# Kernel tuning notes

Hardware: AMD Instinct MI355X
Metric: run time of the kernel (lower is better)

## Reference

```python
import jax, jax.numpy as jnp
import numpy as np

H, L, N1, N2, N3 = 256, 141, 9, 34, 98
B, S = 64, 512

def setup_inputs() -> dict:
    key = jax.random.key(0)
    cnt = [0]
    def nrm(shape, s=0.05):
        cnt[0] += 1
        return jax.random.normal(jax.random.fold_in(key, cnt[0]), shape, jnp.float32) * s
    d = {}
    d['inputs'] = jax.random.randint(jax.random.fold_in(key, 1000), (B, S), 0, 30522)
    d['text_hidden'] = nrm((B, S, 768), 1.0)
    d['label_encoding'] = nrm((L, H), 1.0)
    d['w12'] = (jax.random.uniform(jax.random.fold_in(key, 1001), (N1, N2)) < 0.3).astype(jnp.float32)
    d['w23'] = (jax.random.uniform(jax.random.fold_in(key, 1002), (N2, N3)) < 0.3).astype(jnp.float32)
    d['fre12'] = jax.random.uniform(jax.random.fold_in(key, 1003), (N1, N2), jnp.float32)
    d['fre23'] = jax.random.uniform(jax.random.fold_in(key, 1004), (N2, N3), jnp.float32)
    for name in ['wi1', 'wf1', 'wo1', 'wu1', 'wi2', 'wf2', 'wo2', 'wu2']:
        d[name + '_W'] = nrm((H, H)); d[name + '_b'] = nrm((H,))
    for name in ['ui1', 'uf1', 'uo1', 'uu1', 'ui2', 'uf2', 'uo2', 'uu2']:
        d[name + '_W'] = nrm((H, H))
    d['mix_W'] = nrm((3 * H, H)); d['mix_b'] = nrm((H,))
    d['tt_W'] = nrm((768, H)); d['tt_b'] = nrm((H,))
    d['A'] = nrm((L, L)); d['Wp'] = nrm((H, H))
    d['out_W'] = nrm((L * H, L)); d['out_b'] = nrm((L,))
    return d

def reference(inputs, text_hidden, label_encoding, w12, w23, fre12, fre23,
              wi1_W, wi1_b, wf1_W, wf1_b, wo1_W, wo1_b, wu1_W, wu1_b,
              wi2_W, wi2_b, wf2_W, wf2_b, wo2_W, wo2_b, wu2_W, wu2_b,
              ui1_W, uf1_W, uo1_W, uu1_W, ui2_W, uf2_W, uo2_W, uu2_W,
              mix_W, mix_b, tt_W, tt_b, A, Wp, out_W, out_b):
    sig, tanh = jax.nn.sigmoid, jnp.tanh
    v1 = label_encoding[:N1]          # [N1,H]
    v2 = label_encoding[N1:N1 + N2]   # [N2,H]
    v3 = label_encoding[N1 + N2:]     # [N3,H]
    w21, w32 = w12.T, w23.T
    # --- top-down tree-LSTM (suffix 1) ---
    i11 = sig(v1 @ wi1_W + wi1_b); o11 = sig(v1 @ wo1_W + wo1_b); u11 = tanh(v1 @ wu1_W + wu1_b)
    c11 = i11 * u11; h11 = o11 * tanh(c11)
    h21t = w21 @ h11
    i21 = sig(v2 @ wi1_W + wi1_b + h21t @ ui1_W)
    f21 = sig(v2 @ wf1_W + wf1_b + h21t @ uf1_W)
    o21 = sig(v2 @ wo1_W + wo1_b + h21t @ uo1_W)
    u21 = tanh(v2 @ wu1_W + wu1_b + h21t @ uu1_W)
    c21 = i21 * u21 + f21 * (w21 @ c11); h21 = o21 * tanh(c21)
    h31t = w32 @ h21
    i31 = sig(v3 @ wi1_W + wi1_b + h31t @ ui1_W)
    f31 = sig(v3 @ wf1_W + wf1_b + h31t @ uf1_W)
    o31 = sig(v3 @ wo1_W + wo1_b + h31t @ uo1_W)
    u31 = tanh(v3 @ wu1_W + wu1_b + h31t @ uu1_W)
    c31 = i31 * u31 + f31 * (w32 @ c21); h31 = o31 * tanh(c31)
    # --- bottom-up tree-LSTM (suffix 2) ---
    i32 = sig(v3 @ wi2_W + wi2_b); o32 = sig(v3 @ wo2_W + wo2_b); u32 = tanh(v3 @ wu2_W + wu2_b)
    c32 = i32 * u32; h32 = o32 * tanh(c32)
    h22t = fre23 @ h32
    i22 = sig(v2 @ wi2_W + wi2_b + h22t @ ui2_W)
    f22 = sig((w32 @ v2) @ wf2_W + wf2_b + h32 @ uf2_W)   # [N3,H]
    o22 = sig(v2 @ wo2_W + wo2_b + h22t @ uo2_W)
    u22 = tanh(v2 @ wu2_W + wu2_b + h22t @ uu2_W)
    c22 = i22 * u22 + w23 @ (f22 * c32); h22 = o22 * tanh(c22)
    h12t = fre12 @ h22
    i12 = sig(v1 @ wi2_W + wi2_b + h12t @ ui2_W)
    f12 = sig((w21 @ v1) @ wf2_W + wf2_b + h22 @ uf2_W)   # [N2,H]
    o12 = sig(v1 @ wo2_W + wo2_b + h12t @ uo2_W)
    u12 = tanh(v1 @ wu2_W + wu2_b + h12t @ uu2_W)
    c12 = i12 * u12 + w12 @ (f12 * c22); h12 = o12 * tanh(c12)
    h1 = jnp.concatenate([h11, h12], axis=1)
    h2 = jnp.concatenate([h21, h22], axis=1)
    h3 = jnp.concatenate([h31, h32], axis=1)
    le = jnp.concatenate([h1, h2, h3], axis=0)            # [L,2H]
    temp = jax.nn.relu(A @ label_encoding @ Wp)           # [L,H]
    le = jnp.concatenate([le, temp], axis=1) @ mix_W + mix_b  # [L,H]
    # --- masked cross-attention pooling over text ---
    text = tanh(text_hidden @ tt_W + tt_b)                # [B,S,H]
    att = jnp.einsum('lh,bsh->bls', le, text)             # [B,L,S]
    pad = jnp.where((inputs == 0) | (inputs == 101) | (inputs == 102), -jnp.inf, 0.0).astype(text.dtype)
    att = jax.nn.softmax(att + pad[:, None, :], axis=2)
    features = jnp.einsum('bls,bsh->blh', att, text).reshape(inputs.shape[0], -1)  # [B,L*H]
    return sig(features @ out_W + out_b)                  # [B,L]
```

## Files before the change

kernel.cpp:

```cpp
#include <hip/hip_runtime.h>
#include <math.h>

static constexpr int H = 256, L = 141, N1 = 9, N2 = 34, N3 = 98;
static constexpr int B = 64, S = 512;

typedef __attribute__((ext_vector_type(8))) _Float16 f16x8;
typedef __attribute__((ext_vector_type(4))) float f32x4;

__device__ inline unsigned short f2h(float x) {
    _Float16 h = (_Float16)x;
    return __builtin_bit_cast(unsigned short, h);
}
__device__ inline float sigf(float x) { return 1.f / (1.f + __expf(-x)); }

__device__ inline void gload_lds16(const void* g, void* l) {
    __builtin_amdgcn_global_load_lds(
        (const __attribute__((address_space(1))) void*)g,
        (__attribute__((address_space(3))) void*)l, 16, 0, 0);
}

__device__ inline f16x8 cvt8(float4 lo, float4 hi) {
    union { unsigned int u[4]; f16x8 v; } r;
    r.u[0] = f2h(lo.x) | ((unsigned int)f2h(lo.y) << 16);
    r.u[1] = f2h(lo.z) | ((unsigned int)f2h(lo.w) << 16);
    r.u[2] = f2h(hi.x) | ((unsigned int)f2h(hi.y) << 16);
    r.u[3] = f2h(hi.z) | ((unsigned int)f2h(hi.w) << 16);
    return r.v;
}

__global__ __launch_bounds__(256) void conv_ttW(
    const float* __restrict__ W, unsigned short* __restrict__ Bt)
{
    __shared__ unsigned short Tl[32][257];
    const int t = blockIdx.x, tid = threadIdx.x;
    #pragma unroll
    for (int p = 0; p < 32; p++) {
        int lin = p * 256 + tid;
        int r = lin >> 8, c = lin & 255;
        Tl[r][c] = f2h(W[(long)(t * 32 + r) * 256 + c]);
    }
    __syncthreads();
    unsigned short v[32];
    #pragma unroll
    for (int kin = 0; kin < 32; kin++) v[kin] = Tl[kin][tid];
    uint4* dst = (uint4*)(Bt + ((long)t * 256 + tid) * 32);
    #pragma unroll
    for (int q = 0; q < 4; q++) dst[q] = ((const uint4*)v)[q];
}

__global__ __launch_bounds__(256) void text_gemm2(
    const float* __restrict__ Af,
    const unsigned short* __restrict__ Bt,
    const float* __restrict__ bias,
    unsigned short* __restrict__ outH,
    unsigned short* __restrict__ outHT)
{
    __shared__ unsigned short T[256 * 72];
    const int tid  = threadIdx.x;
    const int wave = tid >> 6, lane = tid & 63;
    const int quad = lane >> 4, l16 = lane & 15;
    const int m0 = blockIdx.x * 64;
    const int wm = (wave & 1) * 32;
    const int wn = (wave >> 1) * 128;

    const float* ap0 = Af + (long)(m0 + wm + l16) * 768 + quad * 8;
    const float* ap1 = ap0 + 16 * 768;
    const unsigned short* bp = Bt + (wn + l16) * 32 + quad * 8;

    f32x4 acc[2][8] = {};
    uint4  br0[8], br1[8];
    float4 ar0[4], ar1[4];

    auto tg_load = [&](int tt, uint4 (&BR)[8], float4 (&AR)[4]) {
        const unsigned short* bq = bp + (long)tt * 8192;
        #pragma unroll
        for (int j = 0; j < 8; j++) BR[j] = *(const uint4*)(bq + j * 512);
        const float* a0 = ap0 + tt * 32;
        const float* a1 = ap1 + tt * 32;
        AR[0] = *(const float4*)a0;
        AR[1] = *(const float4*)(a0 + 4);
        AR[2] = *(const float4*)a1;
        AR[3] = *(const float4*)(a1 + 4);
    };
    auto tg_comp = [&](const uint4 (&BR)[8], const float4 (&AR)[4]) {
        f16x8 a0 = cvt8(AR[0], AR[1]);
        f16x8 a1 = cvt8(AR[2], AR[3]);
        #pragma unroll
        for (int j = 0; j < 8; j++) {
            f16x8 bj = __builtin_bit_cast(f16x8, BR[j]);
            acc[0][j] = __builtin_amdgcn_mfma_f32_16x16x32_f16(a0, bj, acc[0][j], 0, 0, 0);
            acc[1][j] = __builtin_amdgcn_mfma_f32_16x16x32_f16(a1, bj, acc[1][j], 0, 0, 0);
        }
    };

    tg_load(0, br0, ar0);
    #pragma unroll 1
    for (int t = 0; t < 24; t += 2) {
        tg_load(t + 1, br1, ar1);
        tg_comp(br0, ar0);
        if (t + 2 < 24) tg_load(t + 2, br0, ar0);
        tg_comp(br1, ar1);
    }

    float bv[8];
    #pragma unroll
    for (int j = 0; j < 8; j++) bv[j] = bias[wn + j * 16 + l16];

    #pragma unroll
    for (int i = 0; i < 2; i++) {
        #pragma unroll
        for (int j = 0; j < 8; j++) {
            const int mlb = wm + i * 16 + quad * 4;
            const int n   = wn + j * 16 + l16;
            unsigned short hv[4];
            #pragma unroll
            for (int r = 0; r < 4; r++) {
                float v = tanhf(acc[i][j][r] + bv[j]);
                hv[r] = f2h(v);
                outH[(long)(m0 + mlb + r) * 256 + n] = hv[r];
            }
            uint2 p;
            p.x = hv[0] | ((unsigned int)hv[1] << 16);
            p.y = hv[2] | ((unsigned int)hv[3] << 16);
            *(uint2*)&T[n * 72 + mlb] = p;
        }
    }
    __syncthreads();
    {
        const int bb = m0 >> 9, s0 = m0 & 511;
        uint4* dst = (uint4*)&outHT[((long)bb * 256 + tid) * 512 + s0];
        const uint4* src = (const uint4*)&T[tid * 72];
        #pragma unroll
        for (int q = 0; q < 8; q++) dst[q] = src[q];
    }
}

template<int EPI, bool CONVA, int IM>
__global__ __launch_bounds__(256) void gemm_mfma(
    const void* __restrict__ Aptr, int lda, long strA,
    const unsigned short* __restrict__ Bp, int ldb, long strB,
    float* __restrict__ C, int ldc, long strC,
    int M, int N, int K,
    const float* __restrict__ bias,
    const int* __restrict__ tokens,
    unsigned short* __restrict__ outH,
    unsigned short* __restrict__ outHT,
    int kChunk)
{
    __shared__ unsigned short A_s[32 * IM * 32];
    __shared__ unsigned short B_s[128 * 32];
    __shared__ unsigned short T[EPI == 1 ? 128 * 64 : 1];
    const int tid  = threadIdx.x;
    const int wave = tid >> 6, lane = tid & 63;
    const int quad = lane >> 4, l16 = lane & 15;
    const int bz = blockIdx.z;
    const int m0 = blockIdx.y * (32 * IM), n0 = blockIdx.x * 128;
    const int wm = (wave & 1) * (16 * IM), wn = (wave >> 1) * 64;

    long aBase, bBase;
    int kBeg, kEnd;
    if (EPI == 4) { aBase = 0; bBase = 0; kBeg = bz * kChunk; kEnd = kBeg + kChunk; }
    else { aBase = (long)bz * strA; bBase = (long)bz * strB; kBeg = 0; kEnd = K; }

    f32x4 acc[IM][4] = {};

    for (int k0 = kBeg; k0 < kEnd; k0 += 32) {
        if (CONVA) {
            const float* Af = (const float*)Aptr + aBase;
            #pragma unroll
            for (int it = 0; it < IM; it++) {
                int idx = it * 256 + tid;
                int row = idx >> 3, col4 = idx & 7;
                int gm = m0 + row; if (gm > M - 1) gm = M - 1;
                float4 v = *(const float4*)(Af + (long)gm * lda + k0 + col4 * 4);
                unsigned int p0 = f2h(v.x) | ((unsigned int)f2h(v.y) << 16);
                unsigned int p1 = f2h(v.z) | ((unsigned int)f2h(v.w) << 16);
                *(uint2*)&A_s[row * 32 + col4 * 4] = make_uint2(p0, p1);
            }
        } else {
            const unsigned short* Ab = (const unsigned short*)Aptr + aBase;
            #pragma unroll
            for (int t = 0; t < IM / 2; t++) {
                int rowb = wave * (8 * IM) + t * 16;
                int gm = m0 + rowb + (lane >> 2); if (gm > M - 1) gm = M - 1;
                gload_lds16(Ab + (long)gm * lda + k0 + (lane & 3) * 8,
                            &A_s[rowb * 32]);
            }
        }
        #pragma unroll
        for (int t = 0; t < 2; t++) {
            int rowb = wave * 32 + t * 16;
            int gn = n0 + rowb + (lane >> 2); if (gn > N - 1) gn = N - 1;
            gload_lds16(Bp + bBase + (long)gn * ldb + k0 + (lane & 3) * 8,
                        &B_s[rowb * 32]);
        }
        __syncthreads();
        f16x8 a[IM], b[4];
        #pragma unroll
        for (int i = 0; i < IM; i++)
            a[i] = *(const f16x8*)&A_s[(wm + i * 16 + l16) * 32 + quad * 8];
        #pragma unroll
        for (int j = 0; j < 4; j++)
            b[j] = *(const f16x8*)&B_s[(wn + j * 16 + l16) * 32 + quad * 8];
        #pragma unroll
        for (int i = 0; i < IM; i++)
            #pragma unroll
            for (int j = 0; j < 4; j++)
                acc[i][j] = __builtin_amdgcn_mfma_f32_16x16x32_f16(
                    a[i], b[j], acc[i][j], 0, 0, 0);
        __syncthreads();
    }

    #pragma unroll
    for (int i = 0; i < IM; i++) {
        #pragma unroll
        for (int j = 0; j < 4; j++) {
            #pragma unroll
            for (int r = 0; r < 4; r++) {
                int ml = wm + i * 16 + quad * 4 + r;
                int nl = wn + j * 16 + l16;
                int gm = m0 + ml, gn = n0 + nl;
                if (gm >= M || gn >= N) continue;
                float v = acc[i][j][r];
                if (EPI == 1) {
                    v = tanhf(v + bias[gn]);
                    unsigned short hv = f2h(v);
                    outH[(long)gm * ldc + gn] = hv;
                    T[nl * 64 + ml] = hv;
                } else if (EPI == 2) {
                    int tok = tokens[(long)bz * 512 + gn];
                    if (tok == 0 || tok == 101 || tok == 102) v -= 1e30f;
                    C[(long)bz * strC + (long)gm * ldc + gn] = v;
                } else if (EPI == 3) {
                    outH[(long)bz * strC + (long)gm * ldc + gn] = f2h(v);
                } else {
                    C[(long)bz * strC + (long)gm * ldc + gn] = v;
                }
            }
        }
    }
    if (EPI == 1) {
        __syncthreads();
        int bb = m0 >> 9, s0 = m0 & 511;
        int rr = tid >> 1, half = tid & 1;
        const uint4* srcp = (const uint4*)&T[rr * 64 + half * 32];
        uint4* dstp = (uint4*)&outHT[((long)bb * 256 + n0 + rr) * 512 + s0 + half * 32];
        dstp[0] = srcp[0]; dstp[1] = srcp[1]; dstp[2] = srcp[2]; dstp[3] = srcp[3];
    }
}

__global__ __launch_bounds__(256) void transp_t64(
    const float* __restrict__ src, unsigned short* __restrict__ dst,
    int R, int C)
{
    __shared__ unsigned short T[64 * 65];
    const int tid = threadIdx.x;
    const int r0 = blockIdx.x * 64, c0 = blockIdx.y * 64;
    #pragma unroll
    for (int p = 0; p < 16; p++) {
        int lin = p * 256 + tid;
        int r = lin >> 6, c = lin & 63;
        int gc = c0 + c;
        float v = (gc < C) ? src[(long)(r0 + r) * C + gc] : 0.f;
        T[c * 65 + r] = f2h(v);
    }
    __syncthreads();
    #pragma unroll
    for (int p = 0; p < 16; p++) {
        int lin = p * 256 + tid;
        int c = lin >> 6, r = lin & 63;
        if (c0 + c < C)
            dst[(long)(c0 + c) * R + r0 + r] = T[c * 65 + r];
    }
}

__global__ __launch_bounds__(256) void gate_pre(
    const float* __restrict__ le,
    const float* W0, const float* W1, const float* W2, const float* W3,
    const float* W4, const float* W5, const float* W6,
    const float* b0, const float* b1, const float* b2, const float* b3,
    const float* b4, const float* b5, const float* b6,
    float* __restrict__ G)
{
    __shared__ float ls[256];
    __shared__ float red[256];
    const int j = blockIdx.x >> 2, x = blockIdx.x & 3, m = blockIdx.y;
    const int tid = threadIdx.x, nl = tid & 63, ks = tid >> 6, n = x * 64 + nl;
    ls[tid] = le[(long)m * 256 + tid];
    __syncthreads();
    const float *W, *bb;
    switch (j) {
        case 0: W = W0; bb = b0; break;  case 1: W = W1; bb = b1; break;
        case 2: W = W2; bb = b2; break;  case 3: W = W3; bb = b3; break;
        case 4: W = W4; bb = b4; break;  case 5: W = W5; bb = b5; break;
        default: W = W6; bb = b6;
    }
    float a0 = 0, a1 = 0, a2 = 0, a3 = 0;
    for (int k = ks; k + 12 < 256; k += 16) {
        long o = (long)k * 256 + n;
        a0 += ls[k] * W[o];        a1 += ls[k + 4] * W[o + 1024];
        a2 += ls[k + 8] * W[o + 2048]; a3 += ls[k + 12] * W[o + 3072];
    }
    red[tid] = a0 + a1 + a2 + a3;
    __syncthreads();
    if (ks == 0)
        G[((long)j * 141 + m) * 256 + n] =
            red[nl] + red[64 + nl] + red[128 + nl] + red[192 + nl] + bb[n];
}

__global__ __launch_bounds__(256) void pre2(
    const float* __restrict__ A, const float* __restrict__ le,
    const float* __restrict__ w23, const float* __restrict__ w12,
    const float* __restrict__ Wp, const float* __restrict__ wf2_W,
    float* __restrict__ tmpP, float* __restrict__ wv2f, float* __restrict__ wv1f)
{
    __shared__ float cs[141];
    __shared__ float t[256];
    __shared__ float red[256];
    const int x = blockIdx.x, y = blockIdx.y;
    const int tid = threadIdx.x, nl = tid & 63, ks = tid >> 6, n = x * 64 + nl;
    int job, m, K1;
    if (y < 141)      { job = 0; m = y;       K1 = 141; }
    else if (y < 239) { job = 1; m = y - 141; K1 = 34; }
    else              { job = 2; m = y - 239; K1 = 9; }
    if (tid < K1)
        cs[tid] = (job == 0) ? A[(long)m * 141 + tid]
                : (job == 1) ? w23[(long)tid * 98 + m]
                             : w12[(long)tid * 34 + m];
    __syncthreads();
    const float* s1 = (job == 1) ? le + 9 * 256 : le;
    float acc = 0;
    #pragma unroll 4
    for (int k = 0; k < K1; k++) acc += cs[k] * s1[(long)k * 256 + tid];
    t[tid] = acc;
    __syncthreads();
    const float* W = (job == 0) ? Wp : wf2_W;
    float a0 = 0, a1 = 0, a2 = 0, a3 = 0;
    for (int k = ks; k + 12 < 256; k += 16) {
        long o = (long)k * 256 + n;
        a0 += t[k] * W[o];        a1 += t[k + 4] * W[o + 1024];
        a2 += t[k + 8] * W[o + 2048]; a3 += t[k + 12] * W[o + 3072];
    }
    red[tid] = a0 + a1 + a2 + a3;
    __syncthreads();
    if (ks == 0) {
        float tot = red[nl] + red[64 + nl] + red[128 + nl] + red[192 + nl];
        if (job == 0)      tmpP[(long)m * 256 + n] = fmaxf(tot, 0.f);
        else if (job == 1) wv2f[(long)m * 256 + n] = tot;
        else               wv1f[(long)m * 256 + n] = tot;
    }
}

__global__ __launch_bounds__(256) void ew1(
    const float* __restrict__ G, float* __restrict__ h11, float* __restrict__ c11,
    float* __restrict__ h32, float* __restrict__ c32)
{
    int y = blockIdx.x, n = threadIdx.x;
    if (y < 9) {
        int m = y;
        float iv = sigf(G[(0L * 141 + m) * 256 + n]);
        float ov = sigf(G[(2L * 141 + m) * 256 + n]);
        float uv = tanhf(G[(3L * 141 + m) * 256 + n]);
        float cv = iv * uv;
        c11[m * 256 + n] = cv; h11[m * 256 + n] = ov * tanhf(cv);
    } else {
        int r = y - 9, grow = 43 + r;
        float iv = sigf(G[(4L * 141 + grow) * 256 + n]);
        float ov = sigf(G[(5L * 141 + grow) * 256 + n]);
        float uv = tanhf(G[(6L * 141 + grow) * 256 + n]);
        float cv = iv * uv;
        c32[r * 256 + n] = cv; h32[r * 256 + n] = ov * tanhf(cv);
    }
}

__global__ __launch_bounds__(256) void chain_mm(int phase,
    const float* __restrict__ w12, const float* __restrict__ w23,
    const float* __restrict__ fre23, const float* __restrict__ fre12,
    const float* __restrict__ h11, const float* __restrict__ c11,
    const float* __restrict__ h32,
    const float* __restrict__ h21, const float* __restrict__ c21,
    const float* __restrict__ h22,
    const float* __restrict__ wv2f, const float* __restrict__ wv1f,
    const float* __restrict__ wf2_b, const float* __restrict__ uf2_W,
    const float* __restrict__ c32, const float* __restrict__ c22,
    float* __restrict__ h21t, float* __restrict__ c21p,
    float* __restrict__ h22t, float* __restrict__ fcb,
    float* __restrict__ h31t, float* __restrict__ c31p,
    float* __restrict__ h12t, float* __restrict__ fc2b)
{
    __shared__ float cs[256];
    __shared__ float red[256];
    const int x = blockIdx.x, y = blockIdx.y;
    const int tid = threadIdx.x, nl = tid & 63, ks = tid >> 6, n = x * 64 + nl;
    int job, m;
    if (phase == 0) {
        if (y < 34)       { job = 0; m = y; }
        else if (y < 68)  { job = 1; m = y - 34; }
        else if (y < 102) { job = 2; m = y - 68; }
        else              { job = 3; m = y - 102; }
    } else {
        if (y < 98)       { job = 0; m = y; }
        else if (y < 196) { job = 1; m = y - 98; }
        else if (y < 205) { job = 2; m = y - 196; }
        else              { job = 3; m = y - 205; }
    }
    if (job < 3) {
        int K; const float* src; float* dst;
        if (phase == 0) {
            K = (job == 2) ? 98 : 9;
            src = (job == 0) ? h11 : (job == 1) ? c11 : h32;
            dst = (job == 0) ? h21t : (job == 1) ? c21p : h22t;
            if (tid < K)
                cs[tid] = (job == 2) ? fre23[(long)m * 98 + tid]
                                     : w12[(long)tid * 34 + m];
        } else {
            K = 34;
            src = (job == 0) ? h21 : (job == 1) ? c21 : h22;
            dst = (job == 0) ? h31t : (job == 1) ? c31p : h12t;
            if (tid < K)
                cs[tid] = (job == 2) ? fre12[(long)m * 34 + tid]
                                     : w23[(long)tid * 98 + m];
        }
        __syncthreads();
        float a0 = 0;
        for (int k = ks; k < K; k += 4) a0 += cs[k] * src[(long)k * 256 + n];
        red[tid] = a0;
        __syncthreads();
        if (ks == 0)
            dst[(long)m * 256 + n] = red[nl] + red[64 + nl] + red[128 + nl] + red[192 + nl];
    } else {
        const float* row = (phase == 0) ? h32 + m * 256 : h22 + m * 256;
        const float* pre = (phase == 0) ? wv2f : wv1f;
        const float* cm  = (phase == 0) ? c32 : c22;
        float* dst       = (phase == 0) ? fcb : fc2b;
        cs[tid] = row[tid];
        __syncthreads();
        float a0 = 0, a1 = 0, a2 = 0, a3 = 0;
        for (int k = ks; k + 12 < 256; k += 16) {
            long o = (long)k * 256 + n;
            a0 += cs[k] * uf2_W[o];        a1 += cs[k + 4] * uf2_W[o + 1024];
            a2 += cs[k + 8] * uf2_W[o + 2048]; a3 += cs[k + 12] * uf2_W[o + 3072];
        }
        red[tid] = a0 + a1 + a2 + a3;
        __syncthreads();
        if (ks == 0) {
            float tot = red[nl] + red[64 + nl] + red[128 + nl] + red[192 + nl]
                      + pre[(long)m * 256 + n] + wf2_b[n];
            dst[(long)m * 256 + n] = sigf(tot) * cm[(long)m * 256 + n];
        }
    }
}

__global__ __launch_bounds__(256) void lstm_fused(int phase,
    const float* __restrict__ G,
    const float* __restrict__ h21t, const float* __restrict__ c21p,
    const float* __restrict__ h22t, const float* __restrict__ fcb,
    const float* __restrict__ h31t, const float* __restrict__ c31p,
    const float* __restrict__ h12t, const float* __restrict__ fc2b,
    const float* __restrict__ w23, const float* __restrict__ w12,
    const float* __restrict__ ui1, const float* __restrict__ uf1,
    const float* __restrict__ uo1, const float* __restrict__ uu1,
    const float* __restrict__ ui2, const float* __restrict__ uo2,
    const float* __restrict__ uu2,
    float* __restrict__ h21, float* __restrict__ c21,
    float* __restrict__ h22, float* __restrict__ c22,
    float* __restrict__ h31, float* __restrict__ h12)
{
    __shared__ float hs[256];
    __shared__ float cs[128];
    __shared__ float red[1024];
    const int x = blockIdx.x, y = blockIdx.y;
    const int tid = threadIdx.x, nl = tid & 63, ks = tid >> 6, n = x * 64 + nl;
    bool modef; int m, grow, Kx = 0;
    const float *hrow, *U0, *U1, *U2, *U3 = nullptr, *Sx = nullptr, *cmod = nullptr;
    float *ho, *co = nullptr;
    if (phase == 0) {
        if (y < 34) { modef = true;  m = y;      grow = 9 + m;  hrow = h21t;
                      U0 = ui1; U1 = uf1; U2 = uo1; U3 = uu1; cmod = c21p; ho = h21; co = c21; }
        else        { modef = false; m = y - 34; grow = 9 + m;  hrow = h22t;
                      U0 = ui2; U1 = uo2; U2 = uu2; Sx = fcb; Kx = 98; ho = h22; co = c22;
                      if (tid < 98) cs[tid] = w23[(long)m * 98 + tid]; }
    } else {
        if (y < 98) { modef = true;  m = y;      grow = 43 + m; hrow = h31t;
                      U0 = ui1; U1 = uf1; U2 = uo1; U3 = uu1; cmod = c31p; ho = h31; co = nullptr; }
        else        { modef = false; m = y - 98; grow = m;      hrow = h12t;
                      U0 = ui2; U1 = uo2; U2 = uu2; Sx = fc2b; Kx = 34; ho = h12; co = nullptr;
                      if (tid < 34) cs[tid] = w12[(long)m * 34 + tid]; }
    }
    hs[tid] = hrow[(long)m * 256 + tid];
    __syncthreads();
    float a0 = 0, a1 = 0, a2 = 0, a3 = 0;
    if (modef) {
        for (int k = ks; k < 256; k += 4) {
            float xv = hs[k]; long o = (long)k * 256 + n;
            a0 += xv * U0[o]; a1 += xv * U1[o]; a2 += xv * U2[o]; a3 += xv * U3[o];
        }
    } else {
        for (int k = ks; k < 256; k += 4) {
            float xv = hs[k]; long o = (long)k * 256 + n;
            a0 += xv * U0[o]; a1 += xv * U1[o]; a2 += xv * U2[o];
        }
        for (int k = ks; k < Kx; k += 4) a3 += cs[k] * Sx[(long)k * 256 + n];
    }
    red[tid] = a0; red[256 + tid] = a1; red[512 + tid] = a2; red[768 + tid] = a3;
    __syncthreads();
    if (ks == 0) {
        float t0 = 0, t1 = 0, t2 = 0, t3 = 0;
        #pragma unroll
        for (int s2 = 0; s2 < 4; s2++) {
            t0 += red[s2 * 64 + nl];       t1 += red[256 + s2 * 64 + nl];
            t2 += red[512 + s2 * 64 + nl]; t3 += red[768 + s2 * 64 + nl];
        }
        if (modef) {
            float ti = t0 + G[(0L * 141 + grow) * 256 + n];
            float tf = t1 + G[(1L * 141 + grow) * 256 + n];
            float to = t2 + G[(2L * 141 + grow) * 256 + n];
            float tu = t3 + G[(3L * 141 + grow) * 256 + n];
            float cv = sigf(ti) * tanhf(tu) + sigf(tf) * cmod[(long)m * 256 + n];
            ho[(long)m * 256 + n] = sigf(to) * tanhf(cv);
            if (co) co[(long)m * 256 + n] = cv;
        } else {
            float ti = t0 + G[(4L * 141 + grow) * 256 + n];
            float to = t1 + G[(5L * 141 + grow) * 256 + n];
            float tu = t2 + G[(6L * 141 + grow) * 256 + n];
            float cv = sigf(ti) * tanhf(tu) + t3;
            ho[(long)m * 256 + n] = sigf(to) * tanhf(cv);
            if (co) co[(long)m * 256 + n] = cv;
        }
    }
}

__global__ __launch_bounds__(256) void mix_mm(
    const float* __restrict__ h11, const float* __restrict__ h12,
    const float* __restrict__ h21, const float* __restrict__ h22,
    const float* __restrict__ h31, const float* __restrict__ h32,
    const float* __restrict__ tmpP, const float* __restrict__ mix_W,
    const float* __restrict__ mix_b, unsigned short* __restrict__ le_h)
{
    __shared__ float ls[768];
    __shared__ float red[256];
    const int x = blockIdx.x, l = blockIdx.y;
    const int tid = threadIdx.x, nl = tid & 63, ks = tid >> 6, n = x * 64 + nl;
    const float *pa, *pb; int r;
    if (l < 9)       { pa = h11; pb = h12; r = l; }
    else if (l < 43) { pa = h21; pb = h22; r = l - 9; }
    else             { pa = h31; pb = h32; r = l - 43; }
    for (int j = tid; j < 768; j += 256) {
        float v;
        if (j < 256)      v = pa[r * 256 + j];
        else if (j < 512) v = pb[r * 256 + (j - 256)];
        else              v = tmpP[l * 256 + (j - 512)];
        ls[j] = v;
    }
    __syncthreads();
    float a0 = 0, a1 = 0, a2 = 0, a3 = 0;
    for (int k = ks; k + 12 < 768; k += 16) {
        long o = (long)k * 256 + n;
        a0 += ls[k] * mix_W[o];        a1 += ls[k + 4] * mix_W[o + 1024];
        a2 += ls[k + 8] * mix_W[o + 2048]; a3 += ls[k + 12] * mix_W[o + 3072];
    }
    red[tid] = a0 + a1 + a2 + a3;
    __syncthreads();
    if (ks == 0) {
        float tot = red[nl] + red[64 + nl] + red[128 + nl] + red[192 + nl] + mix_b[n];
        le_h[(long)l * 256 + n] = f2h(tot);
    }
}

__global__ __launch_bounds__(256) void softmax512(
    const float* __restrict__ att, unsigned short* __restrict__ atth)
{
    __shared__ float red[256];
    const float* row = att + (long)blockIdx.x * 512;
    unsigned short* orow = atth + (long)blockIdx.x * 512;
    int t = threadIdx.x;
    float a = row[t], b = row[t + 256];
    red[t] = fmaxf(a, b);
    __syncthreads();
    for (int s = 128; s > 0; s >>= 1) {
        if (t < s) red[t] = fmaxf(red[t], red[t + s]);
        __syncthreads();
    }
    float m = red[0];
    __syncthreads();
    float ea = __expf(a - m), eb = __expf(b - m);
    red[t] = ea + eb;
    __syncthreads();
    for (int s = 128; s > 0; s >>= 1) {
        if (t < s) red[t] += red[t + s];
        __syncthreads();
    }
    float inv = 1.f / red[0];
    orow[t] = f2h(ea * inv);
    orow[t + 256] = f2h(eb * inv);
}

__global__ __launch_bounds__(256) void out_final(
    const float* __restrict__ acc, const float* __restrict__ ob,
    float* __restrict__ out, int total, int nz)
{
    int i = blockIdx.x * 256 + threadIdx.x;
    if (i >= total) return;
    float v = ob[i % L];
    #pragma unroll 4
    for (int z = 0; z < nz; z++) v += acc[(long)z * total + i];
    out[i] = sigf(v);
}

extern "C" void kernel_launch(void* const* d_in, const int* in_sizes, int n_in,
                              void* d_out, int out_size, void* d_ws, size_t ws_size,
                              hipStream_t stream)
{
    (void)in_sizes; (void)n_in; (void)out_size; (void)ws_size;
    const int*   inputs      = (const int*)d_in[0];
    const float* text_hidden = (const float*)d_in[1];
    const float* label_enc   = (const float*)d_in[2];
    const float* w12   = (const float*)d_in[3];
    const float* w23   = (const float*)d_in[4];
    const float* fre12 = (const float*)d_in[5];
    const float* fre23 = (const float*)d_in[6];
    const float* wi1_W = (const float*)d_in[7],  *wi1_b = (const float*)d_in[8];
    const float* wf1_W = (const float*)d_in[9],  *wf1_b = (const float*)d_in[10];
    const float* wo1_W = (const float*)d_in[11], *wo1_b = (const float*)d_in[12];
    const float* wu1_W = (const float*)d_in[13], *wu1_b = (const float*)d_in[14];
    const float* wi2_W = (const float*)d_in[15], *wi2_b = (const float*)d_in[16];
    const float* wf2_W = (const float*)d_in[17], *wf2_b = (const float*)d_in[18];
    const float* wo2_W = (const float*)d_in[19], *wo2_b = (const float*)d_in[20];
    const float* wu2_W = (const float*)d_in[21], *wu2_b = (const float*)d_in[22];
    const float* ui1_W = (const float*)d_in[23], *uf1_W = (const float*)d_in[24];
    const float* uo1_W = (const float*)d_in[25], *uu1_W = (const float*)d_in[26];
    const float* ui2_W = (const float*)d_in[27], *uf2_W = (const float*)d_in[28];
    const float* uo2_W = (const float*)d_in[29], *uu2_W = (const float*)d_in[30];
    const float* mix_W = (const float*)d_in[31], *mix_b = (const float*)d_in[32];
    const float* tt_W  = (const float*)d_in[33], *tt_b  = (const float*)d_in[34];
    const float* Amat  = (const float*)d_in[35], *Wp    = (const float*)d_in[36];
    const float* out_W = (const float*)d_in[37], *out_b = (const float*)d_in[38];
    float* out = (float*)d_out;

    float* ws = (float*)d_ws;
    float* att     = ws; ws += (long)B * L * S;
    unsigned short* text_h  = (unsigned short*)ws; ws += (long)B * S * H / 2;
    unsigned short* text_hT = (unsigned short*)ws; ws += (long)B * S * H / 2;
    unsigned short* att_h   = (unsigned short*)ws; ws += (long)B * L * S / 2;
    unsigned short* tt_Wt   = (unsigned short*)ws; ws += 768 * H / 2;
    unsigned short* le_h    = (unsigned short*)ws; ws += L * H / 2 + 4;
    unsigned short* out_Wh  = (unsigned short*)ws; ws += (long)L * 36096 / 2;
    unsigned short* feat_h  = (unsigned short*)ws; ws += (long)B * L * H / 2;
    float* outacc = ws; ws += (long)B * L * 141;
    float* G    = ws; ws += 7 * 141 * 256;
    float* tmpP = ws; ws += L * H;
    float* wv2f = ws; ws += N3 * H;
    float* wv1f = ws; ws += N2 * H;
    float* h11  = ws; ws += N1 * H;  float* c11  = ws; ws += N1 * H;
    float* h21  = ws; ws += N2 * H;  float* c21  = ws; ws += N2 * H;
    float* h21t = ws; ws += N2 * H;  float* c21p = ws; ws += N2 * H;
    float* h31  = ws; ws += N3 * H;  float* h31t = ws; ws += N3 * H;
    float* c31p = ws; ws += N3 * H;
    float* h32  = ws; ws += N3 * H;  float* c32  = ws; ws += N3 * H;
    float* h22  = ws; ws += N2 * H;  float* c22  = ws; ws += N2 * H;
    float* h22t = ws; ws += N2 * H;  float* fcb  = ws; ws += N3 * H;
    float* h12  = ws; ws += N1 * H;  float* h12t = ws; ws += N1 * H;
    float* fc2b = ws; ws += N2 * H;

    conv_ttW<<<24, 256, 0, stream>>>(tt_W, tt_Wt);
    text_gemm2<<<512, 256, 0, stream>>>(
        text_hidden, tt_Wt, tt_b, text_h, text_hT);
    gate_pre<<<dim3(28, 141), 256, 0, stream>>>(label_enc,
        wi1_W, wf1_W, wo1_W, wu1_W, wi2_W, wo2_W, wu2_W,
        wi1_b, wf1_b, wo1_b, wu1_b, wi2_b, wo2_b, wu2_b, G);
    pre2<<<dim3(4, 273), 256, 0, stream>>>(Amat, label_enc, w23, w12, Wp, wf2_W,
        tmpP, wv2f, wv1f);
    transp_t64<<<dim3(36096 / 64, 3), 256, 0, stream>>>(out_W, out_Wh, 36096, 141);
    ew1<<<107, 256, 0, stream>>>(G, h11, c11, h32, c32);
    chain_mm<<<dim3(4, 200), 256, 0, stream>>>(0, w12, w23, fre23, fre12,
        h11, c11, h32, h21, c21, h22, wv2f, wv1f, wf2_b, uf2_W, c32, c22,
        h21t, c21p, h22t, fcb, h31t, c31p, h12t, fc2b);
    lstm_fused<<<dim3(4, 68), 256, 0, stream>>>(0, G,
        h21t, c21p, h22t, fcb, h31t, c31p, h12t, fc2b, w23, w12,
        ui1_W, uf1_W, uo1_W, uu1_W, ui2_W, uo2_W, uu2_W,
        h21, c21, h22, c22, h31, h12);
    chain_mm<<<dim3(4, 239), 256, 0, stream>>>(1, w12, w23, fre23, fre12,
        h11, c11, h32, h21, c21, h22, wv2f, wv1f, wf2_b, uf2_W, c32, c22,
        h21t, c21p, h22t, fcb, h31t, c31p, h12t, fc2b);
    lstm_fused<<<dim3(4, 107), 256, 0, stream>>>(1, G,
        h21t, c21p, h22t, fcb, h31t, c31p, h12t, fc2b, w23, w12,
        ui1_W, uf1_W, uo1_W, uu1_W, ui2_W, uo2_W, uu2_W,
        h21, c21, h22, c22, h31, h12);
    mix_mm<<<dim3(4, 141), 256, 0, stream>>>(h11, h12, h21, h22, h31, h32,
        tmpP, mix_W, mix_b, le_h);
    gemm_mfma<2, false, 2><<<dim3(S / 128, (L + 63) / 64, B), 256, 0, stream>>>(
        le_h, H, 0, text_h, H, (long)S * H, att, S, (long)L * S,
        L, S, H, nullptr, inputs, nullptr, nullptr, 0);
    softmax512<<<B * L, 256, 0, stream>>>(att, att_h);
    gemm_mfma<3, false, 2><<<dim3(H / 128, (L + 63) / 64, B), 256, 0, stream>>>(
        att_h, S, (long)L * S, text_hT, S, (long)H * S, nullptr, H, (long)L * H,
        L, H, S, nullptr, nullptr, feat_h, nullptr, 0);
    gemm_mfma<4, false, 2><<<dim3(2, 1, 141), 256, 0, stream>>>(
        feat_h, L * H, 0, out_Wh, L * H, 0, outacc, L, (long)B * L,
        B, L, L * H, nullptr, nullptr, nullptr, nullptr, 256);
    out_final<<<(B * L + 255) / 256, 256, 0, stream>>>(outacc, out_b, out, B * L, 141);
}
```

Before: 482.0 us.

## Rewrite text projection GEMM with LDS staging and async B prefetch

Replaces the register-only text_gemm2 with text_gemm3, which uses 512 threads in 8 waves. A is converted to fp16 and written into double-buffered swizzled LDS, and B is streamed into a triple-buffered LDS ring with global_load_lds. The goal is to cut redundant per-wave global loads of B and A, and to overlap memory traffic with MFMA work through explicit waitcnt and barrier pipelining. In exchange it adds barriers every k-step and hand-tuned vmcnt counts that are fragile, and it reduces the per-wave tile.

```diff
diff --git a/kernel.cpp b/kernel.cpp
--- a/kernel.cpp
+++ b/kernel.cpp
@@ -19,15 +19,6 @@
         (__attribute__((address_space(3))) void*)l, 16, 0, 0);
 }
 
-__device__ inline f16x8 cvt8(float4 lo, float4 hi) {
-    union { unsigned int u[4]; f16x8 v; } r;
-    r.u[0] = f2h(lo.x) | ((unsigned int)f2h(lo.y) << 16);
-    r.u[1] = f2h(lo.z) | ((unsigned int)f2h(lo.w) << 16);
-    r.u[2] = f2h(hi.x) | ((unsigned int)f2h(hi.y) << 16);
-    r.u[3] = f2h(hi.z) | ((unsigned int)f2h(hi.w) << 16);
-    return r.v;
-}
-
 __global__ __launch_bounds__(256) void conv_ttW(
     const float* __restrict__ W, unsigned short* __restrict__ Bt)
 {
@@ -48,68 +39,117 @@
     for (int q = 0; q < 4; q++) dst[q] = ((const uint4*)v)[q];
 }
 
-__global__ __launch_bounds__(256) void text_gemm2(
+__global__ __launch_bounds__(512, 4) void text_gemm3(
     const float* __restrict__ Af,
     const unsigned short* __restrict__ Bt,
     const float* __restrict__ bias,
     unsigned short* __restrict__ outH,
     unsigned short* __restrict__ outHT)
 {
-    __shared__ unsigned short T[256 * 72];
+    __shared__ unsigned short smem[28672];
+    unsigned short* As = smem;
+    unsigned short* Bs = smem + 4096;
+    unsigned short* T  = smem;
+
     const int tid  = threadIdx.x;
     const int wave = tid >> 6, lane = tid & 63;
     const int quad = lane >> 4, l16 = lane & 15;
     const int m0 = blockIdx.x * 64;
-    const int wm = (wave & 1) * 32;
-    const int wn = (wave >> 1) * 128;
-
-    const float* ap0 = Af + (long)(m0 + wm + l16) * 768 + quad * 8;
-    const float* ap1 = ap0 + 16 * 768;
-    const unsigned short* bp = Bt + (wn + l16) * 32 + quad * 8;
-
-    f32x4 acc[2][8] = {};
-    uint4  br0[8], br1[8];
-    float4 ar0[4], ar1[4];
-
-    auto tg_load = [&](int tt, uint4 (&BR)[8], float4 (&AR)[4]) {
-        const unsigned short* bq = bp + (long)tt * 8192;
-        #pragma unroll
-        for (int j = 0; j < 8; j++) BR[j] = *(const uint4*)(bq + j * 512);
-        const float* a0 = ap0 + tt * 32;
-        const float* a1 = ap1 + tt * 32;
-        AR[0] = *(const float4*)a0;
-        AR[1] = *(const float4*)(a0 + 4);
-        AR[2] = *(const float4*)a1;
-        AR[3] = *(const float4*)(a1 + 4);
+    const int wm = (wave >> 2) * 32;
+    const int wn = (wave & 3) * 64;
+
+    const int arow = tid >> 3;
+    const int ac16 = tid & 7;
+    const float* aSrc = Af + (long)(m0 + arow) * 768 + ac16 * 4;
+    const int ac8d = ac16 ^ ((arow & 3) << 1);
+    const int aWoff = arow * 32 + ac8d * 4;
+
+    const int bsc = (lane & 3) ^ ((lane >> 3) & 3);
+    const long bSrcOff0 = (long)(wave * 32 + (lane >> 2)) * 32 + bsc * 8;
+    const long bSrcOff1 = bSrcOff0 + 16 * 32;
+    const int bDst0 = (wave * 32) * 32, bDst1 = (wave * 32 + 16) * 32;
+
+    int aro[2], bro[4];
+    #pragma unroll
+    for (int i = 0; i < 2; i++) {
+        int r = wm + i * 16 + l16;
+        aro[i] = r * 32 + ((quad * 2) ^ ((r & 3) << 1)) * 4;
+    }
+    #pragma unroll
+    for (int j = 0; j < 4; j++) {
+        int n = wn + j * 16 + l16;
+        bro[j] = n * 32 + ((quad ^ ((n >> 1) & 3)) << 3);
+    }
+
+    f32x4 acc[2][4] = {};
+    float4 ar0, ar1;
+
+    auto issueB = [&](int kt, int pb) {
+        const unsigned short* src = Bt + (long)kt * 8192;
+        unsigned short* d = Bs + pb * 8192;
+        gload_lds16(src + bSrcOff0, d + bDst0);
+        gload_lds16(src + bSrcOff1, d + bDst1);
     };
-    auto tg_comp = [&](const uint4 (&BR)[8], const float4 (&AR)[4]) {
-        f16x8 a0 = cvt8(AR[0], AR[1]);
-        f16x8 a1 = cvt8(AR[2], AR[3]);
-        #pragma unroll
-        for (int j = 0; j < 8; j++) {
-            f16x8 bj = __builtin_bit_cast(f16x8, BR[j]);
-            acc[0][j] = __builtin_amdgcn_mfma_f32_16x16x32_f16(a0, bj, acc[0][j], 0, 0, 0);
-            acc[1][j] = __builtin_amdgcn_mfma_f32_16x16x32_f16(a1, bj, acc[1][j], 0, 0, 0);
-        }
+    auto writeA = [&](const float4& v, int pa) {
+        unsigned int p0 = f2h(v.x) | ((unsigned int)f2h(v.y) << 16);
+        unsigned int p1 = f2h(v.z) | ((unsigned int)f2h(v.w) << 16);
+        *(uint2*)&As[pa * 2048 + aWoff] = make_uint2(p0, p1);
     };
 
-    tg_load(0, br0, ar0);
+    ar0 = *(const float4*)(aSrc + 0 * 32);
+    issueB(0, 0);
+    ar1 = *(const float4*)(aSrc + 1 * 32);
+    issueB(1, 1);
+    asm volatile("s_waitcnt vmcnt(5)" ::: "memory");
+    writeA(ar0, 0);
+    asm volatile("s_waitcnt vmcnt(3)" ::: "memory");
+    asm volatile("s_waitcnt lgkmcnt(0)" ::: "memory");
+    asm volatile("s_barrier" ::: "memory");
+
+    auto body = [&](int t, float4& arIn, float4& arOut, int pa, int pr) {
+        int kt2 = (t + 2 <= 23) ? t + 2 : 23;
+        arOut = *(const float4*)(aSrc + kt2 * 32);
+        f16x8 a[2], b[4];
+        const unsigned short* ab = As + pa * 2048;
+        const unsigned short* bb = Bs + pr * 8192;
+        #pragma unroll
+        for (int i = 0; i < 2; i++) a[i] = *(const f16x8*)&ab[aro[i]];
+        #pragma unroll
+        for (int j = 0; j < 4; j++) b[j] = *(const f16x8*)&bb[bro[j]];
+        #pragma unroll
+        for (int i = 0; i < 2; i++)
+            #pragma unroll
+            for (int j = 0; j < 4; j++)
+                acc[i][j] = __builtin_amdgcn_mfma_f32_16x16x32_f16(
+                    a[i], b[j], acc[i][j], 0, 0, 0);
+        asm volatile("s_waitcnt vmcnt(3)" ::: "memory");
+        writeA(arIn, pa ^ 1);
+        int pw = pr + 2; if (pw >= 3) pw -= 3;
+        issueB(kt2, pw);
+        asm volatile("s_waitcnt vmcnt(3)" ::: "memory");
+        asm volatile("s_waitcnt lgkmcnt(0)" ::: "memory");
+        asm volatile("s_barrier" ::: "memory");
+    };
+
+    int pr = 0;
     #pragma unroll 1
     for (int t = 0; t < 24; t += 2) {
-        tg_load(t + 1, br1, ar1);
-        tg_comp(br0, ar0);
-        if (t + 2 < 24) tg_load(t + 2, br0, ar0);
-        tg_comp(br1, ar1);
-    }
-
-    float bv[8];
-    #pragma unroll
-    for (int j = 0; j < 8; j++) bv[j] = bias[wn + j * 16 + l16];
+        body(t,     ar1, ar0, t & 1 ? 1 : 0, pr);
+        int pr1 = pr + 1; if (pr1 >= 3) pr1 -= 3;
+        body(t + 1, ar0, ar1, 1, pr1);
+        pr = pr1 + 1; if (pr >= 3) pr -= 3;
+    }
+    asm volatile("s_waitcnt vmcnt(0)" ::: "memory");
+    __syncthreads();
+
+    float bv[4];
+    #pragma unroll
+    for (int j = 0; j < 4; j++) bv[j] = bias[wn + j * 16 + l16];
 
     #pragma unroll
     for (int i = 0; i < 2; i++) {
         #pragma unroll
-        for (int j = 0; j < 8; j++) {
+        for (int j = 0; j < 4; j++) {
             const int mlb = wm + i * 16 + quad * 4;
             const int n   = wn + j * 16 + l16;
             unsigned short hv[4];
@@ -127,11 +167,12 @@
     }
     __syncthreads();
     {
-        const int bb = m0 >> 9, s0 = m0 & 511;
-        uint4* dst = (uint4*)&outHT[((long)bb * 256 + tid) * 512 + s0];
-        const uint4* src = (const uint4*)&T[tid * 72];
-        #pragma unroll
-        for (int q = 0; q < 8; q++) dst[q] = src[q];
+        const int bb2 = m0 >> 9, s0 = m0 & 511;
+        const int n = tid >> 1, half = tid & 1;
+        const uint4* src = (const uint4*)&T[n * 72 + half * 32];
+        uint4* dst = (uint4*)&outHT[((long)bb2 * 256 + n) * 512 + s0 + half * 32];
+        dst[0] = src[0]; dst[1] = src[1];
+        dst[2] = src[2]; dst[3] = src[3];
     }
 }
 
@@ -663,7 +704,7 @@
     float* fc2b = ws; ws += N2 * H;
 
     conv_ttW<<<24, 256, 0, stream>>>(tt_W, tt_Wt);
-    text_gemm2<<<512, 256, 0, stream>>>(
+    text_gemm3<<<512, 512, 0, stream>>>(
         text_hidden, tt_Wt, tt_b, text_h, text_hT);
     gate_pre<<<dim3(28, 141), 256, 0, stream>>>(label_enc,
         wi1_W, wf1_W, wo1_W, wu1_W, wi2_W, wo2_W, wu2_W,
```

Result: faster. 462.6 us (-4.0%).
